# Kernel optimization log

Hardware: AMD Instinct MI355X
Metric: run time of the kernel (lower is better)

The kernel has to match this reference:

```python
import jax, jax.numpy as jnp
import numpy as np

N_HEADS = 16
N_KV_HEADS = 4
HEAD_DIM = 128
D_MODEL = 2048
WINDOW = 1024
THETA = 10000.0
EPS = 1e-6


def _rmsnorm(x, w):
    var = jnp.mean(x * x, axis=-1, keepdims=True)
    return x * jax.lax.rsqrt(var + EPS) * w


def _rope(x, pos):
    # x: [B, H, S, D]; rotate-half (llama-style) RoPE
    d2 = HEAD_DIM // 2
    inv_freq = 1.0 / (THETA ** (jnp.arange(0, HEAD_DIM, 2, dtype=jnp.float32) / HEAD_DIM))
    ang = pos[:, None].astype(jnp.float32) * inv_freq[None, :]  # [S, D/2]
    cos = jnp.cos(ang)[None, None]
    sin = jnp.sin(ang)[None, None]
    x1, x2 = x[..., :d2], x[..., d2:]
    return jnp.concatenate([x1 * cos - x2 * sin, x1 * sin + x2 * cos], axis=-1)


def setup_inputs() -> dict:
    key = jax.random.key(0)
    ks = jax.random.split(key, 7)
    B, S = 1, 2048
    s = 0.02
    return {
        "x": jax.random.normal(ks[0], (B, S, D_MODEL), jnp.float32),
        "wq": jax.random.normal(ks[1], (N_HEADS * HEAD_DIM, D_MODEL), jnp.float32) * s,
        "wk": jax.random.normal(ks[2], (N_KV_HEADS * HEAD_DIM, D_MODEL), jnp.float32) * s,
        "wv": jax.random.normal(ks[3], (N_KV_HEADS * HEAD_DIM, D_MODEL), jnp.float32) * s,
        "wo": jax.random.normal(ks[4], (D_MODEL, N_HEADS * HEAD_DIM), jnp.float32) * s,
        "q_norm_w": jnp.ones((HEAD_DIM,), jnp.float32),
        "k_norm_w": jnp.ones((HEAD_DIM,), jnp.float32),
    }


def reference(x, wq, wk, wv, wo, q_norm_w, k_norm_w):
    B, S, _ = x.shape
    past_length = 0
    scale = HEAD_DIM ** -0.5
    n_rep = N_HEADS // N_KV_HEADS

    q = (x @ wq.T).reshape(B, S, N_HEADS, HEAD_DIM).transpose(0, 2, 1, 3)
    k = (x @ wk.T).reshape(B, S, N_KV_HEADS, HEAD_DIM).transpose(0, 2, 1, 3)
    v = (x @ wv.T).reshape(B, S, N_KV_HEADS, HEAD_DIM).transpose(0, 2, 1, 3)

    q = _rmsnorm(q, q_norm_w)
    k = _rmsnorm(k, k_norm_w)

    pos = jnp.arange(S) + past_length
    q = _rope(q, pos)
    k = _rope(k, pos)

    # GQA: materialize repeated KV heads, as in _repeat_kv
    k_rep = jnp.repeat(k, n_rep, axis=1)  # [B, H, S, D]
    v_rep = jnp.repeat(v, n_rep, axis=1)

    # sliding-window causal mask (total_seq_len=S > WINDOW)
    q_idx = jnp.arange(S)[:, None] + past_length
    k_idx = jnp.arange(S)[None, :]
    mask = (q_idx >= k_idx) & (q_idx - k_idx < WINDOW)  # [S, S]

    scores = jnp.einsum("bhqd,bhkd->bhqk", q, k_rep) * scale
    scores = jnp.where(mask[None, None], scores, jnp.float32(-jnp.inf))
    attn = jax.nn.softmax(scores, axis=-1)
    out = jnp.einsum("bhqk,bhkd->bhqd", attn, v_rep)

    out = out.transpose(0, 2, 1, 3).reshape(B, S, N_HEADS * HEAD_DIM)
    return out @ wo.T
```

## Files before the change

kernel.cpp:

```cpp
#include <hip/hip_runtime.h>
#include <hip/hip_bf16.h>
#include <cstdint>
#include <cstddef>

typedef __attribute__((ext_vector_type(4))) float f32x4;
typedef __attribute__((ext_vector_type(8))) short bf16x8;
typedef __attribute__((ext_vector_type(8))) unsigned short us8;

#define MFMA16(a, b, c) __builtin_amdgcn_mfma_f32_16x16x32_bf16(a, b, c, 0, 0, 0)

__device__ inline unsigned short f2bf(float f) {
    unsigned int u = __float_as_uint(f);
    u += 0x7fffu + ((u >> 16) & 1u);
    return (unsigned short)(u >> 16);
}
__device__ inline float bf2f(unsigned short u) {
    return __uint_as_float((unsigned int)u << 16);
}

__device__ inline void gload_lds16(const void* g, void* l) {
    __builtin_amdgcn_global_load_lds(
        (const __attribute__((address_space(1))) void*)g,
        (__attribute__((address_space(3))) void*)l, 16, 0, 0);
}
__device__ inline unsigned lds_addr(const void* p) {
    return (unsigned)(size_t)((__attribute__((address_space(3))) const void*)p);
}

__global__ __launch_bounds__(256) void prep_all(const float* __restrict__ x,
                                                const float* __restrict__ wq,
                                                const float* __restrict__ wk,
                                                const float* __restrict__ wv,
                                                const float* __restrict__ wo,
                                                unsigned short* __restrict__ xb,
                                                unsigned short* __restrict__ wqkv,
                                                unsigned short* __restrict__ wob,
                                                float2* __restrict__ tbl) {
    const int b = blockIdx.x;
    if (b < 14336) {
        const float* src; unsigned short* dst; int off4;
        if (b < 4096)       { src = x;  dst = xb;                 off4 = b; }
        else if (b < 8192)  { src = wq; dst = wqkv;               off4 = b - 4096; }
        else if (b < 9216)  { src = wk; dst = wqkv + 2048 * 2048; off4 = b - 8192; }
        else if (b < 10240) { src = wv; dst = wqkv + 2560 * 2048; off4 = b - 9216; }
        else                { src = wo; dst = wob;                off4 = b - 10240; }
        int i = (off4 * 256 + threadIdx.x) * 4;
        float4 v = *(const float4*)(src + i);
        ushort4 o;
        o.x = f2bf(v.x); o.y = f2bf(v.y); o.z = f2bf(v.z); o.w = f2bf(v.w);
        *(ushort4*)(dst + i) = o;
    } else {
        int idx = (b - 14336) * 256 + threadIdx.x;
        int row = idx >> 6, t = idx & 63;
        float inv_freq = exp2f((float)t * (-2.0f / 128.0f) * 13.287712379549449f);
        float s, c;
        sincosf((float)row * inv_freq, &s, &c);
        tbl[idx] = make_float2(c, s);
    }
}

__global__ __launch_bounds__(512, 2) void gemm256(const unsigned short* __restrict__ A,
                                                  const unsigned short* __restrict__ B,
                                                  float* __restrict__ Cp,
                                                  int M, int N, int Kfull, int kspan) {
    __shared__ unsigned short As[3][8192];
    __shared__ unsigned short Bs[3][8192];
    const int tid = threadIdx.x;
    const int lane = tid & 63, wave = tid >> 6;
    const int wr = wave >> 2, wc = wave & 3;
    const int l15 = lane & 15, l4 = lane >> 4;
    const int gx = gridDim.x;
    const int nwg = gx * gridDim.y;
    const int bid0 = blockIdx.y * gx + blockIdx.x;
    const int q8 = nwg >> 3, r8 = nwg & 7;
    const int xcd = bid0 & 7, sub = bid0 >> 3;
    const int wgid = ((xcd < r8) ? xcd * (q8 + 1) : r8 * (q8 + 1) + (xcd - r8) * q8) + sub;
    const int bm = wgid / gx, bn = wgid % gx;
    const int z = blockIdx.z;
    const unsigned short* Az = A + (size_t)z * kspan;
    const unsigned short* Bz = B + (size_t)z * kspan;
    float* C = Cp + (size_t)z * M * N;
    const int nK = kspan >> 5;

    f32x4 acc[8][4] = {};

    const int r0 = tid >> 2, qs = tid & 3;
    const int qsw = qs ^ ((r0 >> 1) & 3);
    const unsigned short* pa0 = Az + (size_t)(bm * 256 + r0) * Kfull + qsw * 8;
    const unsigned short* pa1 = pa0 + (size_t)128 * Kfull;
    const unsigned short* pb0 = Bz + (size_t)(bn * 256 + r0) * Kfull + qsw * 8;
    const unsigned short* pb1 = pb0 + (size_t)128 * Kfull;

#define STG(kt, bb)                                            \
    do {                                                       \
        gload_lds16(pa0 + (kt) * 32, &As[bb][tid * 8]);        \
        gload_lds16(pa1 + (kt) * 32, &As[bb][4096 + tid * 8]); \
        gload_lds16(pb0 + (kt) * 32, &Bs[bb][tid * 8]);        \
        gload_lds16(pb1 + (kt) * 32, &Bs[bb][4096 + tid * 8]); \
    } while (0)

    const int q = l4 ^ ((l15 >> 1) & 3);
    const unsigned aB = lds_addr(&As[0][0]) + (unsigned)((wr * 128 + l15) * 64 + q * 16);
    const unsigned bB = lds_addr(&Bs[0][0]) + (unsigned)((wc * 64 + l15) * 64 + q * 16);

#define DSR(dst, addr, off) \
    asm volatile("ds_read_b128 %0, %1 offset:" #off : "=v"(dst) : "v"(addr))

    STG(0, 0);
    STG(1, 1);
    int bc = 0, bs = 2;
    for (int kt = 0; kt < nK; ++kt) {
        if (kt + 1 < nK)
            asm volatile("s_waitcnt vmcnt(4)\ns_barrier" ::: "memory");
        else
            asm volatile("s_waitcnt vmcnt(0)\ns_barrier" ::: "memory");
        __builtin_amdgcn_sched_barrier(0);

        bf16x8 a[8], b[4];
        {
            const unsigned aA = aB + bc * 16384;
            const unsigned bA = bB + bc * 16384;
            DSR(a[0], aA, 0);    DSR(a[1], aA, 1024);
            DSR(a[2], aA, 2048); DSR(a[3], aA, 3072);
            DSR(a[4], aA, 4096); DSR(a[5], aA, 5120);
            DSR(a[6], aA, 6144); DSR(a[7], aA, 7168);
            DSR(b[0], bA, 0);    DSR(b[1], bA, 1024);
            DSR(b[2], bA, 2048); DSR(b[3], bA, 3072);
        }
        if (kt + 2 < nK) STG(kt + 2, bs);
        asm volatile("s_waitcnt lgkmcnt(0)" ::: "memory");
        __builtin_amdgcn_sched_barrier(0);

        __builtin_amdgcn_s_setprio(1);
#pragma unroll
        for (int m = 0; m < 8; ++m)
#pragma unroll
            for (int n = 0; n < 4; ++n)
                acc[m][n] = MFMA16(a[m], b[n], acc[m][n]);
        __builtin_amdgcn_s_setprio(0);

        if (++bc == 3) bc = 0;
        if (++bs == 3) bs = 0;
    }
#undef STG
#undef DSR

    for (int m = 0; m < 8; ++m)
        for (int n = 0; n < 4; ++n)
            for (int j = 0; j < 4; ++j) {
                int row = bm * 256 + wr * 128 + m * 16 + l4 * 4 + j;
                int col = bn * 256 + wc * 64 + n * 16 + l15;
                C[(size_t)row * N + col] = acc[m][n][j];
            }
}

__global__ __launch_bounds__(256) void norm_rope(const float* __restrict__ p0,
                                                 const float* __restrict__ p1,
                                                 const float* __restrict__ qw,
                                                 const float* __restrict__ kw,
                                                 const float2* __restrict__ tbl,
                                                 unsigned short* __restrict__ Qb,
                                                 unsigned short* __restrict__ Kb,
                                                 unsigned short* __restrict__ Vb) {
    const int row = blockIdx.x;
    const int head = blockIdx.y * 4 + (threadIdx.x >> 6);
    const int t = threadIdx.x & 63;
    const size_t off = (size_t)row * 3072 + head * 128;
    float x1 = p0[off + t] + p1[off + t];
    float x2 = p0[off + t + 64] + p1[off + t + 64];
    if (head < 20) {
        float ss = x1 * x1 + x2 * x2;
        for (int m = 32; m; m >>= 1) ss += __shfl_xor(ss, m);
        float r = rsqrtf(ss * (1.0f / 128.0f) + 1e-6f);
        const float* w = (head < 16) ? qw : kw;
        float y1 = x1 * r * w[t], y2 = x2 * r * w[t + 64];
        float2 cs = tbl[row * 64 + t];
        x1 = y1 * cs.x - y2 * cs.y;
        x2 = y1 * cs.y + y2 * cs.x;
    }
    unsigned short* dst;
    if (head < 16)      dst = Qb + ((size_t)head * 2048 + row) * 128;
    else if (head < 20) dst = Kb + ((size_t)(head - 16) * 2048 + row) * 128;
    else                dst = Vb + ((size_t)(head - 20) * 2048 + row) * 128;
    dst[t] = f2bf(x1);
    dst[t + 64] = f2bf(x2);
}

__global__ __launch_bounds__(256) void transpose_v(const unsigned short* __restrict__ Vb,
                                                   unsigned short* __restrict__ VbT) {
    const int kt = blockIdx.x;
    const int h  = blockIdx.y;
    __shared__ unsigned short T[64 * 130];
    const int tid = threadIdx.x;
    for (int i = 0; i < 4; ++i) {
        int s = i * 256 + tid;
        int r = s >> 4, c = (s & 15) * 8;
        us8 v = *(const us8*)(Vb + ((size_t)h * 2048 + kt * 64 + r) * 128 + c);
        for (int j = 0; j < 8; ++j) T[r * 130 + c + j] = v[j];
    }
    __syncthreads();
    for (int i = 0; i < 4; ++i) {
        int s = i * 256 + tid;
        int d = s >> 3, ck = (s & 7) * 8;
        us8 v;
        for (int j = 0; j < 8; ++j) v[j] = T[(ck + j) * 130 + d];
        *(us8*)(VbT + (size_t)h * 128 * 2048 + (size_t)d * 2048 + kt * 64 + ck) = v;
    }
}

__global__ __launch_bounds__(256) void attn_fwd(const unsigned short* __restrict__ Qb,
                                                const unsigned short* __restrict__ Kb,
                                                const unsigned short* __restrict__ VbT,
                                                unsigned short* __restrict__ Ob) {
    const int qt = blockIdx.x;
    const int h = blockIdx.y;
    const int kvh = h >> 2;
    const int q0 = qt * 64;
    __shared__ unsigned short Ks[2][64 * 128];
    __shared__ unsigned short Vs[2][128 * 64];
    __shared__ unsigned short Ps[4][16 * 72];
    const int tid = threadIdx.x;
    const int lane = tid & 63, wave = tid >> 6;
    const int l15 = lane & 15, l4 = lane >> 4;

    bf16x8 qf[4];
    {
        const unsigned short* qrow =
            Qb + ((size_t)h * 2048 + q0 + wave * 16 + l15) * 128 + l4 * 8;
        for (int kk = 0; kk < 4; ++kk) qf[kk] = *(const bf16x8*)(qrow + kk * 32);
    }
    f32x4 o[8] = {};
    float m2[4], lp[4];
    for (int j = 0; j < 4; ++j) { m2[j] = -1e30f; lp[j] = 0.0f; }
    const float SCALE2 = 0.08838834764831843f * 1.4426950408889634f;
    const int kt_lo = (qt >= 16) ? (qt - 16) : 0;

    const unsigned short* Kh = Kb + (size_t)kvh * 2048 * 128;
    const unsigned short* Vh = VbT + (size_t)kvh * 128 * 2048;

    {
        const int kt = kt_lo;
        for (int i = 0; i < 4; ++i) {
            int s = i * 256 + tid;
            int r = s >> 4;
            int cb = ((s & 15) * 16) ^ ((r & 7) << 4);
            gload_lds16(Kh + (size_t)(kt * 64 + r) * 128 + (cb >> 1), &Ks[0][s * 8]);
        }
        for (int i = 0; i < 4; ++i) {
            int s = i * 256 + tid;
            int d = s >> 3;
            int cb = ((s & 7) * 16) ^ ((d & 7) << 4);
            gload_lds16(Vh + (size_t)d * 2048 + kt * 64 + (cb >> 1), &Vs[0][s * 8]);
        }
    }

    int cur = 0;
    for (int kt = kt_lo; kt <= qt; ++kt) {
        __syncthreads();

        if (kt < qt) {
            const int kn = kt + 1;
            for (int i = 0; i < 4; ++i) {
                int s = i * 256 + tid;
                int r = s >> 4;
                int cb = ((s & 15) * 16) ^ ((r & 7) << 4);
                gload_lds16(Kh + (size_t)(kn * 64 + r) * 128 + (cb >> 1), &Ks[cur ^ 1][s * 8]);
            }
            for (int i = 0; i < 4; ++i) {
                int s = i * 256 + tid;
                int d = s >> 3;
                int cb = ((s & 7) * 16) ^ ((d & 7) << 4);
                gload_lds16(Vh + (size_t)d * 2048 + kn * 64 + (cb >> 1), &Vs[cur ^ 1][s * 8]);
            }
        }

        f32x4 s[4] = {};
        __builtin_amdgcn_s_setprio(1);
        for (int nn = 0; nn < 4; ++nn)
            for (int kk = 0; kk < 4; ++kk) {
                int r = nn * 16 + l15;
                int cb = (kk * 64 + l4 * 16) ^ ((r & 7) << 4);
                bf16x8 kf = *(const bf16x8*)((const char*)&Ks[cur][0] + r * 256 + cb);
                s[nn] = MFMA16(qf[kk], kf, s[nn]);
            }
        __builtin_amdgcn_s_setprio(0);

        float p[4][4];
        const bool masked = (kt == qt) || (qt >= 16 && kt == kt_lo);
        if (masked) {
            for (int nn = 0; nn < 4; ++nn) {
                int kc = kt * 64 + nn * 16 + l15;
                for (int j = 0; j < 4; ++j) {
                    int qr = q0 + wave * 16 + l4 * 4 + j;
                    float sv = s[nn][j] * SCALE2;
                    bool ok = (qr >= kc) && (qr - kc < 1024);
                    p[nn][j] = ok ? sv : -1e30f;
                }
            }
        } else {
            for (int nn = 0; nn < 4; ++nn)
                for (int j = 0; j < 4; ++j) p[nn][j] = s[nn][j] * SCALE2;
        }

        float mx4[4];
        bool flag = true;
        for (int j = 0; j < 4; ++j) {
            float mx = fmaxf(fmaxf(p[0][j], p[1][j]), fmaxf(p[2][j], p[3][j]));
            for (int mk = 8; mk; mk >>= 1) mx = fmaxf(mx, __shfl_xor(mx, mk));
            mx4[j] = mx;
            flag = flag && (mx <= m2[j] + 11.0f);
        }
        if (!__all(flag)) {
            for (int j = 0; j < 4; ++j) {
                float mnew = fmaxf(m2[j], mx4[j]);
                float corr = exp2f(m2[j] - mnew);
                m2[j] = mnew;
                lp[j] *= corr;
                for (int dd = 0; dd < 8; ++dd) o[dd][j] *= corr;
            }
        }
        for (int j = 0; j < 4; ++j) {
            float rs = 0.0f;
            for (int nn = 0; nn < 4; ++nn) {
                float pv = exp2f(p[nn][j] - m2[j]);
                p[nn][j] = pv;
                rs += pv;
            }
            lp[j] += rs;
        }

        for (int j = 0; j < 4; ++j)
            for (int nn = 0; nn < 4; ++nn)
                Ps[wave][(l4 * 4 + j) * 72 + nn * 16 + l15] = f2bf(p[nn][j]);

        bf16x8 pa[2];
        for (int kk2 = 0; kk2 < 2; ++kk2)
            pa[kk2] = *(const bf16x8*)&Ps[wave][l15 * 72 + kk2 * 32 + l4 * 8];

        __builtin_amdgcn_s_setprio(1);
        for (int dd = 0; dd < 8; ++dd)
            for (int kk2 = 0; kk2 < 2; ++kk2) {
                int d = dd * 16 + l15;
                int cb = (kk2 * 64 + l4 * 16) ^ ((d & 7) << 4);
                bf16x8 vf = *(const bf16x8*)((const char*)&Vs[cur][0] + d * 128 + cb);
                o[dd] = MFMA16(pa[kk2], vf, o[dd]);
            }
        __builtin_amdgcn_s_setprio(0);
        cur ^= 1;
    }

    for (int j = 0; j < 4; ++j) {
        float lt = lp[j];
        for (int mk = 8; mk; mk >>= 1) lt += __shfl_xor(lt, mk);
        float inv = 1.0f / lt;
        int row = q0 + wave * 16 + l4 * 4 + j;
        unsigned short* orow = Ob + (size_t)row * 2048 + h * 128;
        for (int dd = 0; dd < 8; ++dd) orow[dd * 16 + l15] = f2bf(o[dd][j] * inv);
    }
}

__global__ __launch_bounds__(256) void add4(const float* __restrict__ p,
                                            float* __restrict__ out, int n) {
    int i = (blockIdx.x * 256 + threadIdx.x) * 4;
    if (i >= n) return;
    f32x4 a = *(const f32x4*)(p + i);
    f32x4 b = *(const f32x4*)(p + 4194304 + i);
    f32x4 c = *(const f32x4*)(p + 8388608 + i);
    f32x4 d = *(const f32x4*)(p + 12582912 + i);
    a = (a + b) + (c + d);
    *(f32x4*)(out + i) = a;
}

extern "C" void kernel_launch(void* const* d_in, const int* in_sizes, int n_in,
                              void* d_out, int out_size, void* d_ws, size_t ws_size,
                              hipStream_t stream) {
    const float* x  = (const float*)d_in[0];
    const float* wq = (const float*)d_in[1];
    const float* wk = (const float*)d_in[2];
    const float* wv = (const float*)d_in[3];
    const float* wo = (const float*)d_in[4];
    const float* qw = (const float*)d_in[5];
    const float* kw = (const float*)d_in[6];
    float* out = (float*)d_out;

    char* ws = (char*)d_ws;
    unsigned short* xb   = (unsigned short*)(ws + 0);
    unsigned short* wqkv = (unsigned short*)(ws + 8388608);
    unsigned short* wob  = (unsigned short*)(ws + 20971520);
    float*          qkvP = (float*)(ws + 29360128);
    unsigned short* Qb   = (unsigned short*)(ws + 79691776);
    unsigned short* Kb   = (unsigned short*)(ws + 88080384);
    unsigned short* Vb   = (unsigned short*)(ws + 90177536);
    unsigned short* VbT  = (unsigned short*)(ws + 92274688);
    float*          outP = (float*)(ws + 29360128);
    unsigned short* Ob   = (unsigned short*)(ws + 96468992);
    float2*         tbl  = (float2*)(ws + 104857600);

    prep_all<<<dim3(14848), dim3(256), 0, stream>>>(x, wq, wk, wv, wo, xb, wqkv, wob, tbl);
    gemm256<<<dim3(12, 8, 2), dim3(512), 0, stream>>>(xb, wqkv, qkvP, 2048, 3072, 2048, 1024);
    norm_rope<<<dim3(2048, 6), dim3(256), 0, stream>>>(qkvP, qkvP + 2048 * 3072, qw, kw, tbl, Qb, Kb, Vb);
    transpose_v<<<dim3(32, 4), dim3(256), 0, stream>>>(Vb, VbT);
    attn_fwd<<<dim3(32, 16), dim3(256), 0, stream>>>(Qb, Kb, VbT, Ob);
    gemm256<<<dim3(8, 8, 4), dim3(512), 0, stream>>>(Ob, wob, outP, 2048, 2048, 2048, 512);
    add4<<<dim3(4096), dim3(256), 0, stream>>>(outP, out, 2048 * 2048);
}
```

Before: 147.7 us.

## Fuse V split-K reduction into transpose, fold softmax scale into Q, remap attention grid

The transpose kernel now reads V directly from the two split-K fp32 partials, sums them and converts to bf16. This removes the separate Vb write and read along with the sixth norm_rope grid column. The softmax scale times log2(e) is folded into Q during norm_rope, so the attention inner loop skips a multiply per score. The mask test becomes a single unsigned compare, and the cross-lane max reduction only runs when a rescale is needed. Attention blocks are remapped through a 1D grid that interleaves heads, and bf16 conversion uses the hardware packed-convert instruction, which changes rounding behaviour slightly.

After: 143.7 us. 2.7% less time.

```diff
diff --git a/kernel.cpp b/kernel.cpp
--- a/kernel.cpp
+++ b/kernel.cpp
@@ -14,8 +14,10 @@
     u += 0x7fffu + ((u >> 16) & 1u);
     return (unsigned short)(u >> 16);
 }
-__device__ inline float bf2f(unsigned short u) {
-    return __uint_as_float((unsigned int)u << 16);
+__device__ inline unsigned short f2bf_fast(float f) {
+    float r;
+    asm("v_cvt_pk_bf16_f32 %0, %1, %2" : "=v"(r) : "v"(f), "v"(f));
+    return (unsigned short)__float_as_uint(r);
 }
 
 __device__ inline void gload_lds16(const void* g, void* l) {
@@ -160,50 +162,55 @@
                                                  const float* __restrict__ kw,
                                                  const float2* __restrict__ tbl,
                                                  unsigned short* __restrict__ Qb,
-                                                 unsigned short* __restrict__ Kb,
-                                                 unsigned short* __restrict__ Vb) {
+                                                 unsigned short* __restrict__ Kb) {
     const int row = blockIdx.x;
     const int head = blockIdx.y * 4 + (threadIdx.x >> 6);
     const int t = threadIdx.x & 63;
     const size_t off = (size_t)row * 3072 + head * 128;
     float x1 = p0[off + t] + p1[off + t];
     float x2 = p0[off + t + 64] + p1[off + t + 64];
-    if (head < 20) {
-        float ss = x1 * x1 + x2 * x2;
-        for (int m = 32; m; m >>= 1) ss += __shfl_xor(ss, m);
-        float r = rsqrtf(ss * (1.0f / 128.0f) + 1e-6f);
-        const float* w = (head < 16) ? qw : kw;
-        float y1 = x1 * r * w[t], y2 = x2 * r * w[t + 64];
-        float2 cs = tbl[row * 64 + t];
-        x1 = y1 * cs.x - y2 * cs.y;
-        x2 = y1 * cs.y + y2 * cs.x;
-    }
-    unsigned short* dst;
-    if (head < 16)      dst = Qb + ((size_t)head * 2048 + row) * 128;
-    else if (head < 20) dst = Kb + ((size_t)(head - 16) * 2048 + row) * 128;
-    else                dst = Vb + ((size_t)(head - 20) * 2048 + row) * 128;
+    float ss = x1 * x1 + x2 * x2;
+    for (int m = 32; m; m >>= 1) ss += __shfl_xor(ss, m);
+    float r = rsqrtf(ss * (1.0f / 128.0f) + 1e-6f);
+    const float* w = (head < 16) ? qw : kw;
+    float y1 = x1 * r * w[t], y2 = x2 * r * w[t + 64];
+    float2 cs = tbl[row * 64 + t];
+    x1 = y1 * cs.x - y2 * cs.y;
+    x2 = y1 * cs.y + y2 * cs.x;
+    if (head < 16) {
+        const float SCALE2 = 0.12751879526654698f;
+        x1 *= SCALE2; x2 *= SCALE2;
+    }
+    unsigned short* dst = (head < 16) ? Qb + ((size_t)head * 2048 + row) * 128
+                                      : Kb + ((size_t)(head - 16) * 2048 + row) * 128;
     dst[t] = f2bf(x1);
     dst[t + 64] = f2bf(x2);
 }
 
-__global__ __launch_bounds__(256) void transpose_v(const unsigned short* __restrict__ Vb,
+__global__ __launch_bounds__(256) void transpose_v(const float* __restrict__ p0,
+                                                   const float* __restrict__ p1,
                                                    unsigned short* __restrict__ VbT) {
     const int kt = blockIdx.x;
     const int h  = blockIdx.y;
-    __shared__ unsigned short T[64 * 130];
+    __shared__ unsigned short T[64 * 132];
     const int tid = threadIdx.x;
-    for (int i = 0; i < 4; ++i) {
+    for (int i = 0; i < 8; ++i) {
         int s = i * 256 + tid;
-        int r = s >> 4, c = (s & 15) * 8;
-        us8 v = *(const us8*)(Vb + ((size_t)h * 2048 + kt * 64 + r) * 128 + c);
-        for (int j = 0; j < 8; ++j) T[r * 130 + c + j] = v[j];
+        int r = s >> 5, c = (s & 31) * 4;
+        size_t off = (size_t)(kt * 64 + r) * 3072 + (20 + h) * 128 + c;
+        float4 a = *(const float4*)(p0 + off);
+        float4 b = *(const float4*)(p1 + off);
+        ushort4 o;
+        o.x = f2bf(a.x + b.x); o.y = f2bf(a.y + b.y);
+        o.z = f2bf(a.z + b.z); o.w = f2bf(a.w + b.w);
+        *(ushort4*)&T[r * 132 + c] = o;
     }
     __syncthreads();
     for (int i = 0; i < 4; ++i) {
         int s = i * 256 + tid;
         int d = s >> 3, ck = (s & 7) * 8;
         us8 v;
-        for (int j = 0; j < 8; ++j) v[j] = T[(ck + j) * 130 + d];
+        for (int j = 0; j < 8; ++j) v[j] = T[(ck + j) * 132 + d];
         *(us8*)(VbT + (size_t)h * 128 * 2048 + (size_t)d * 2048 + kt * 64 + ck) = v;
     }
 }
@@ -212,8 +219,10 @@
                                                 const unsigned short* __restrict__ Kb,
                                                 const unsigned short* __restrict__ VbT,
                                                 unsigned short* __restrict__ Ob) {
-    const int qt = blockIdx.x;
-    const int h = blockIdx.y;
+    const int bid = blockIdx.x;
+    const int seq = bid >> 3;
+    const int h = (bid & 7) * 2 + (seq >> 5);
+    const int qt = seq & 31;
     const int kvh = h >> 2;
     const int q0 = qt * 64;
     __shared__ unsigned short Ks[2][64 * 128];
@@ -232,7 +241,6 @@
     f32x4 o[8] = {};
     float m2[4], lp[4];
     for (int j = 0; j < 4; ++j) { m2[j] = -1e30f; lp[j] = 0.0f; }
-    const float SCALE2 = 0.08838834764831843f * 1.4426950408889634f;
     const int kt_lo = (qt >= 16) ? (qt - 16) : 0;
 
     const unsigned short* Kh = Kb + (size_t)kvh * 2048 * 128;
@@ -292,27 +300,26 @@
                 int kc = kt * 64 + nn * 16 + l15;
                 for (int j = 0; j < 4; ++j) {
                     int qr = q0 + wave * 16 + l4 * 4 + j;
-                    float sv = s[nn][j] * SCALE2;
-                    bool ok = (qr >= kc) && (qr - kc < 1024);
-                    p[nn][j] = ok ? sv : -1e30f;
+                    unsigned diff = (unsigned)(qr - kc);
+                    p[nn][j] = (diff < 1024u) ? s[nn][j] : -1e30f;
                 }
             }
         } else {
             for (int nn = 0; nn < 4; ++nn)
-                for (int j = 0; j < 4; ++j) p[nn][j] = s[nn][j] * SCALE2;
-        }
-
-        float mx4[4];
+                for (int j = 0; j < 4; ++j) p[nn][j] = s[nn][j];
+        }
+
+        float mxl[4];
         bool flag = true;
         for (int j = 0; j < 4; ++j) {
-            float mx = fmaxf(fmaxf(p[0][j], p[1][j]), fmaxf(p[2][j], p[3][j]));
-            for (int mk = 8; mk; mk >>= 1) mx = fmaxf(mx, __shfl_xor(mx, mk));
-            mx4[j] = mx;
-            flag = flag && (mx <= m2[j] + 11.0f);
+            mxl[j] = fmaxf(fmaxf(p[0][j], p[1][j]), fmaxf(p[2][j], p[3][j]));
+            flag = flag && (mxl[j] <= m2[j] + 11.0f);
         }
         if (!__all(flag)) {
             for (int j = 0; j < 4; ++j) {
-                float mnew = fmaxf(m2[j], mx4[j]);
+                float mx = mxl[j];
+                for (int mk = 8; mk; mk >>= 1) mx = fmaxf(mx, __shfl_xor(mx, mk));
+                float mnew = fmaxf(m2[j], mx);
                 float corr = exp2f(m2[j] - mnew);
                 m2[j] = mnew;
                 lp[j] *= corr;
@@ -331,7 +338,7 @@
 
         for (int j = 0; j < 4; ++j)
             for (int nn = 0; nn < 4; ++nn)
-                Ps[wave][(l4 * 4 + j) * 72 + nn * 16 + l15] = f2bf(p[nn][j]);
+                Ps[wave][(l4 * 4 + j) * 72 + nn * 16 + l15] = f2bf_fast(p[nn][j]);
 
         bf16x8 pa[2];
         for (int kk2 = 0; kk2 < 2; ++kk2)
@@ -355,7 +362,7 @@
         float inv = 1.0f / lt;
         int row = q0 + wave * 16 + l4 * 4 + j;
         unsigned short* orow = Ob + (size_t)row * 2048 + h * 128;
-        for (int dd = 0; dd < 8; ++dd) orow[dd * 16 + l15] = f2bf(o[dd][j] * inv);
+        for (int dd = 0; dd < 8; ++dd) orow[dd * 16 + l15] = f2bf_fast(o[dd][j] * inv);
     }
 }
 
@@ -390,7 +397,6 @@
     float*          qkvP = (float*)(ws + 29360128);
     unsigned short* Qb   = (unsigned short*)(ws + 79691776);
     unsigned short* Kb   = (unsigned short*)(ws + 88080384);
-    unsigned short* Vb   = (unsigned short*)(ws + 90177536);
     unsigned short* VbT  = (unsigned short*)(ws + 92274688);
     float*          outP = (float*)(ws + 29360128);
     unsigned short* Ob   = (unsigned short*)(ws + 96468992);
@@ -398,9 +404,9 @@
 
     prep_all<<<dim3(14848), dim3(256), 0, stream>>>(x, wq, wk, wv, wo, xb, wqkv, wob, tbl);
     gemm256<<<dim3(12, 8, 2), dim3(512), 0, stream>>>(xb, wqkv, qkvP, 2048, 3072, 2048, 1024);
-    norm_rope<<<dim3(2048, 6), dim3(256), 0, stream>>>(qkvP, qkvP + 2048 * 3072, qw, kw, tbl, Qb, Kb, Vb);
-    transpose_v<<<dim3(32, 4), dim3(256), 0, stream>>>(Vb, VbT);
-    attn_fwd<<<dim3(32, 16), dim3(256), 0, stream>>>(Qb, Kb, VbT, Ob);
+    norm_rope<<<dim3(2048, 5), dim3(256), 0, stream>>>(qkvP, qkvP + 2048 * 3072, qw, kw, tbl, Qb, Kb);
+    transpose_v<<<dim3(32, 4), dim3(256), 0, stream>>>(qkvP, qkvP + 2048 * 3072, VbT);
+    attn_fwd<<<dim3(512), dim3(256), 0, stream>>>(Qb, Kb, VbT, Ob);
     gemm256<<<dim3(8, 8, 4), dim3(512), 0, stream>>>(Ob, wob, outP, 2048, 2048, 2048, 512);
     add4<<<dim3(4096), dim3(256), 0, stream>>>(outP, out, 2048 * 2048);
 }
```
